# Kernel optimization log

Hardware: AMD Instinct MI355X
Metric: run time of the kernel (lower is better)

The kernel has to match this reference:

```python
import jax, jax.numpy as jnp
import numpy as np

K = 4096   # infeatures
N = 11008  # outfeatures
T = 8192   # tokens (batch*seq)
GROUP = 32
E8M0_BIAS = 127
E2M1_VALS = jnp.array([0.0, 0.5, 1.0, 1.5, 2.0, 3.0, 4.0, 6.0], dtype=jnp.float32)


def setup_inputs() -> dict:
    key = jax.random.key(0)
    k1, k2, k3, k4 = jax.random.split(key, 4)
    x = jax.random.normal(k1, (T, K), dtype=jnp.float32)
    # packed fp4: 8 nibbles per int32 along the in-feature axis -> [K//8, N]
    weight_packed = jax.random.randint(k2, (K // 8, N), 0, 2147483647, dtype=jnp.int32)
    # e8m0 exponents near the bias so 2^(e-127) stays well-conditioned in fp32
    weight_scale_e8m0 = 112 + jax.random.randint(k3, (K // GROUP, N), 0, 30, dtype=jnp.int32)
    bias = jax.random.normal(k4, (N,), dtype=jnp.float32)
    return {"x": x, "weight_packed": weight_packed,
            "weight_scale_e8m0": weight_scale_e8m0, "bias": bias}


def dequantize_weight(weight_packed, weight_scale_e8m0):
    # unpack 8 fp4 nibbles per int32: nibble j -> in-feature row r*8 + j
    shifts = (jnp.arange(8, dtype=jnp.int32) * 4)[None, :, None]       # [1,8,1]
    nib = (weight_packed[:, None, :] >> shifts) & 0xF                   # [K//8,8,N]
    mag = E2M1_VALS[nib & 0x7]                                           # e2m1 magnitude
    sign = jnp.where((nib >> 3) & 1 == 1, -1.0, 1.0).astype(jnp.float32)
    w = (mag * sign).reshape(K, N)
    # per-group e8m0 scale: 2^(e - 127), groups of 32 along in-features
    scale = jnp.exp2((weight_scale_e8m0 - E8M0_BIAS).astype(jnp.float32))  # [K//32,N]
    w = (w.reshape(K // GROUP, GROUP, N) * scale[:, None, :]).reshape(K, N)
    return w


def reference(x, weight_packed, weight_scale_e8m0, bias):
    w = dequantize_weight(weight_packed, weight_scale_e8m0)  # [K, N]
    return x @ w + bias                                       # [T, N]
```

## Files before the change

kernel.cpp:

```cpp
#include <hip/hip_runtime.h>


#define TDIM 8192
#define KDIM 4096
#define NDIM 11008

typedef __attribute__((ext_vector_type(8))) short short8;
typedef __attribute__((ext_vector_type(8))) unsigned short ushort8;
typedef __attribute__((ext_vector_type(4))) float f32x4;

__device__ __forceinline__ unsigned short f2bf(float f) {
    unsigned int u = __float_as_uint(f);
    u += 0x7FFFu + ((u >> 16) & 1u);
    return (unsigned short)(u >> 16);
}

__device__ __forceinline__ unsigned short nib2bf(unsigned int v, int e) {
    unsigned int m3 = v & 7u;
    if (m3 == 0u) return 0;
    unsigned int s = (v & 8u) << 12;
    unsigned int E = (unsigned int)e + (m3 >> 1) - 1u;
    unsigned int man = (m3 >= 2u) ? ((m3 & 1u) << 6) : 0u;
    return (unsigned short)(s | (E << 7) | man);
}

__device__ __forceinline__ void gload_lds16(const void* g, void* l) {
    __builtin_amdgcn_global_load_lds(
        (const __attribute__((address_space(1))) void*)g,
        (__attribute__((address_space(3))) void*)l, 16, 0, 0);
}

__global__ __launch_bounds__(256) void convert_x(const float* __restrict__ x,
                                                 unsigned short* __restrict__ xbf) {
    size_t i = ((size_t)blockIdx.x * 256 + threadIdx.x) * 8;
    float4 v0 = *(const float4*)(x + i);
    float4 v1 = *(const float4*)(x + i + 4);
    ushort8 r;
    r[0] = f2bf(v0.x); r[1] = f2bf(v0.y); r[2] = f2bf(v0.z); r[3] = f2bf(v0.w);
    r[4] = f2bf(v1.x); r[5] = f2bf(v1.y); r[6] = f2bf(v1.z); r[7] = f2bf(v1.w);
    *(ushort8*)(xbf + i) = r;
}

__global__ __launch_bounds__(256) void dequant_w(const int* __restrict__ wp,
                                                 const int* __restrict__ wse,
                                                 unsigned short* __restrict__ wt) {
    __shared__ int sT[64][65];
    const int tid = threadIdx.x;
    const int n0 = blockIdx.x * 64;
    const int r0 = blockIdx.y * 64;

    #pragma unroll
    for (int i = 0; i < 16; ++i) {
        int idx = i * 256 + tid;
        int r = idx >> 6, n = idx & 63;
        sT[r][n] = wp[(size_t)(r0 + r) * NDIM + n0 + n];
    }
    __syncthreads();
    #pragma unroll
    for (int i = 0; i < 16; ++i) {
        int idx = i * 256 + tid;
        int n = idx >> 6, r = idx & 63;
        unsigned int p = (unsigned int)sT[r][n];
        int e = wse[(size_t)((r0 + r) >> 2) * NDIM + n0 + n];
        ushort8 o;
        #pragma unroll
        for (int j = 0; j < 8; ++j) o[j] = nib2bf((p >> (4 * j)) & 0xFu, e);
        *(ushort8*)(wt + (size_t)(n0 + n) * KDIM + (size_t)(r0 + r) * 8) = o;
    }
}

__global__ __launch_bounds__(512, 1) void gemm256(const unsigned short* __restrict__ xbf,
                                                  const unsigned short* __restrict__ wt,
                                                  const float* __restrict__ bias,
                                                  float* __restrict__ out) {
    __shared__ __attribute__((aligned(16))) unsigned short lds[2][2][16384];
    const int tid = threadIdx.x;
    const int l = tid & 63, wid = tid >> 6;
    const int wm = wid >> 2, wn = wid & 3;

    {
    }
    int b = blockIdx.x;
    int swz = (b & 7) * 172 + (b >> 3);
    int band = swz / 344;
    int r = swz % 344;
    int st = r >> 5; if (st > 10) st = 10;
    int ii = r - (st << 5);
    int w = (st < 10) ? 4 : 3;
    const int bm0 = (band * 8 + ii / w) * 256;
    const int bn0 = (st * 4 + ii % w) * 256;

    int r_s[2], k_s[2];
    #pragma unroll
    for (int j = 0; j < 2; ++j) {
        int chunk = j * 512 + wid * 64 + l;
        int sr = chunk >> 6;
        int cin = chunk & 63;
        cin ^= ((cin >> 5) & 1) << 1;
        r_s[j] = sr * 16 + (cin >> 2);
        k_s[j] = (cin & 3) * 8;
    }

    f32x4 acc[8][4] = {};
    short8 afr[4], bfr[4];

    auto stage = [&](int s) {
        int tau = s >> 2;
        int idx = s & 3;
        int mat = idx & 1, hk = idx >> 1, c = tau & 1;
        const unsigned short* base = mat ? wt : xbf;
        int rb = mat ? bn0 : bm0;
        int kb = tau * 64 + hk * 32;
        #pragma unroll
        for (int j = 0; j < 2; ++j) {
            const unsigned short* src = base + (size_t)(rb + r_s[j]) * KDIM + kb + k_s[j];
            unsigned short* dst = &lds[c][mat][hk * 8192 + (j * 512 + wid * 64) * 8];
            gload_lds16(src, dst);
        }
    };

    #pragma unroll
    for (int s = 0; s < 6; ++s) stage(s);
    asm volatile("s_waitcnt vmcnt(4)" ::: "memory");
    __builtin_amdgcn_s_barrier();

    #pragma unroll 2
    for (int t = 0; t < 64; ++t) {
        const unsigned short* tA = &lds[t & 1][0][0];
        const unsigned short* tB = &lds[t & 1][1][0];
        #pragma unroll
        for (int p = 0; p < 4; ++p) {
            const int ks = p >> 1, mh = p & 1;
            if (mh == 0) {
                #pragma unroll
                for (int nf = 0; nf < 4; ++nf) {
                    int byte = ks * 16384 + (wn * 4 + nf) * 1024 + (l & 15) * 64 + ((l >> 4) << 4);
                    byte ^= (l & 8) << 2;
                    bfr[nf] = *(const short8*)((const char*)tB + byte);
                }
            }
            #pragma unroll
            for (int i = 0; i < 4; ++i) {
                int byte = ks * 16384 + (wm * 8 + mh * 4 + i) * 1024 + (l & 15) * 64 + ((l >> 4) << 4);
                byte ^= (l & 8) << 2;
                afr[i] = *(const short8*)((const char*)tA + byte);
            }
            int s = 4 * t + p + 6;
            if (s < 256) stage(s);
            __builtin_amdgcn_s_barrier();
            asm volatile("s_waitcnt lgkmcnt(0)" ::: "memory");
            __builtin_amdgcn_s_setprio(1);
            #pragma unroll
            for (int i = 0; i < 4; ++i)
                #pragma unroll
                for (int nf = 0; nf < 4; ++nf)
                    acc[mh * 4 + i][nf] = __builtin_amdgcn_mfma_f32_16x16x32_bf16(
                        afr[i], bfr[nf], acc[mh * 4 + i][nf], 0, 0, 0);
            __builtin_amdgcn_s_setprio(0);
            if (p == 3) {
                if (t < 62) asm volatile("s_waitcnt vmcnt(4)" ::: "memory");
                else        asm volatile("s_waitcnt vmcnt(0)" ::: "memory");
            }
            __builtin_amdgcn_s_barrier();
        }
    }

    const int crow = (l >> 4) * 4, ccol = l & 15;
    #pragma unroll
    for (int nf = 0; nf < 4; ++nf) {
        int col = bn0 + wn * 64 + nf * 16 + ccol;
        float bv = bias[col];
        #pragma unroll
        for (int m = 0; m < 8; ++m) {
            int row0 = bm0 + wm * 128 + m * 16 + crow;
            #pragma unroll
            for (int j2 = 0; j2 < 4; ++j2)
                __builtin_nontemporal_store(acc[m][nf][j2] + bv,
                                            &out[(size_t)(row0 + j2) * NDIM + col]);
        }
    }
}

__global__ __launch_bounds__(256, 2) void gemm_fused(const float* __restrict__ x,
                                                     const int* __restrict__ wp,
                                                     const int* __restrict__ wse,
                                                     const float* __restrict__ bias,
                                                     float* __restrict__ out) {
    __shared__ __attribute__((aligned(16))) unsigned short lA[128 * 64];
    __shared__ __attribute__((aligned(16))) unsigned short lB[128 * 64];
    const int tid = threadIdx.x;
    const int l = tid & 63, wid = tid >> 6;
    const int bn0 = blockIdx.x * 128, bm0 = blockIdx.y * 128;
    const int wm = wid >> 1, wn = wid & 1;

    f32x4 acc[4][4] = {};

    for (int k0 = 0; k0 < KDIM; k0 += 64) {
        float4 av0[4], av1[4];
        unsigned int bp[4];
        int be[4];
        #pragma unroll
        for (int i = 0; i < 4; ++i) {
            int seg = i * 256 + tid;
            int row = seg >> 3, kseg = seg & 7;
            const float4* p = (const float4*)(x + (size_t)(bm0 + row) * KDIM + k0 + kseg * 8);
            av0[i] = p[0]; av1[i] = p[1];
        }
        #pragma unroll
        for (int i = 0; i < 4; ++i) {
            int idx = i * 256 + tid;
            int ln = idx & 127, lr = idx >> 7;
            bp[i] = ((const unsigned int*)wp)[(size_t)(k0 / 8 + lr) * NDIM + bn0 + ln];
            be[i] = wse[(size_t)((k0 + lr * 8) >> 5) * NDIM + bn0 + ln];
        }
        #pragma unroll
        for (int i = 0; i < 4; ++i) {
            int seg = i * 256 + tid;
            int row = seg >> 3, kseg = seg & 7;
            ushort8 r;
            r[0] = f2bf(av0[i].x); r[1] = f2bf(av0[i].y); r[2] = f2bf(av0[i].z); r[3] = f2bf(av0[i].w);
            r[4] = f2bf(av1[i].x); r[5] = f2bf(av1[i].y); r[6] = f2bf(av1[i].z); r[7] = f2bf(av1[i].w);
            *(ushort8*)&lA[row * 64 + kseg * 8] = r;
        }
        #pragma unroll
        for (int i = 0; i < 4; ++i) {
            int idx = i * 256 + tid;
            int ln = idx & 127, lr = idx >> 7;
            unsigned int p = bp[i];
            int e = be[i];
            ushort8 r;
            #pragma unroll
            for (int j = 0; j < 8; ++j) r[j] = nib2bf((p >> (4 * j)) & 0xFu, e);
            *(ushort8*)&lB[ln * 64 + lr * 8] = r;
        }
        __syncthreads();
        #pragma unroll
        for (int kc = 0; kc < 2; ++kc) {
            short8 a[4], b[4];
            #pragma unroll
            for (int f = 0; f < 4; ++f) {
                a[f] = *(const short8*)&lA[(wm * 64 + f * 16 + (l & 15)) * 64 + kc * 32 + (l >> 4) * 8];
                b[f] = *(const short8*)&lB[(wn * 64 + f * 16 + (l & 15)) * 64 + kc * 32 + (l >> 4) * 8];
            }
            #pragma unroll
            for (int fm = 0; fm < 4; ++fm)
                #pragma unroll
                for (int fn = 0; fn < 4; ++fn)
                    acc[fm][fn] = __builtin_amdgcn_mfma_f32_16x16x32_bf16(a[fm], b[fn], acc[fm][fn], 0, 0, 0);
        }
        __syncthreads();
    }

    const int crow = (l >> 4) * 4, ccol = l & 15;
    #pragma unroll
    for (int fn = 0; fn < 4; ++fn) {
        int col = bn0 + wn * 64 + fn * 16 + ccol;
        float bv = bias[col];
        #pragma unroll
        for (int fm = 0; fm < 4; ++fm) {
            int row0 = bm0 + wm * 64 + fm * 16 + crow;
            #pragma unroll
            for (int j = 0; j < 4; ++j)
                out[(size_t)(row0 + j) * NDIM + col] = acc[fm][fn][j] + bv;
        }
    }
}

extern "C" void kernel_launch(void* const* d_in, const int* in_sizes, int n_in,
                              void* d_out, int out_size, void* d_ws, size_t ws_size,
                              hipStream_t stream) {
    (void)in_sizes; (void)n_in; (void)out_size;
    const float* x = (const float*)d_in[0];
    const int* wp = (const int*)d_in[1];
    const int* wse = (const int*)d_in[2];
    const float* bias = (const float*)d_in[3];
    float* out = (float*)d_out;

    const size_t xbf_bytes = (size_t)TDIM * KDIM * 2;
    const size_t wt_bytes = (size_t)NDIM * KDIM * 2;

    if (ws_size >= xbf_bytes + wt_bytes) {
        unsigned short* xbf = (unsigned short*)d_ws;
        unsigned short* wt = (unsigned short*)((char*)d_ws + xbf_bytes);
        hipLaunchKernelGGL(convert_x, dim3((TDIM * KDIM) / (256 * 8)), dim3(256), 0, stream, x, xbf);
        hipLaunchKernelGGL(dequant_w, dim3(NDIM / 64, (KDIM / 8) / 64), dim3(256), 0, stream, wp, wse, wt);
        hipLaunchKernelGGL(gemm256, dim3((NDIM / 256) * (TDIM / 256)), dim3(512), 0, stream, xbf, wt, bias, out);
    } else {
        hipLaunchKernelGGL(gemm_fused, dim3(NDIM / 128, TDIM / 128), dim3(256), 0, stream, x, wp, wse, bias, out);
    }
}
```

Measured before the change: 737.6 us.

## Double-buffer MFMA fragments in registers to overlap LDS reads with compute

Restructures the main GEMM loop so LDS fragment reads for the next MFMA cluster are issued while the current cluster runs, using ping-pong A/B register fragments. It also cuts the barriers from two per sub-step to two per K-tile and prefetches the next tile's first fragments before the loop-end barrier. This aims to hide LDS latency and reduce synchronization stalls, at the cost of more VGPRs and a more delicate ordering of waitcnt and barriers against the async global-to-LDS stages.

```diff
diff --git a/kernel.cpp b/kernel.cpp
--- a/kernel.cpp
+++ b/kernel.cpp
@@ -78,8 +78,6 @@
     const int l = tid & 63, wid = tid >> 6;
     const int wm = wid >> 2, wn = wid & 3;
 
-    {
-    }
     int b = blockIdx.x;
     int swz = (b & 7) * 172 + (b >> 3);
     int band = swz / 344;
@@ -102,9 +100,10 @@
     }
 
     f32x4 acc[8][4] = {};
-    short8 afr[4], bfr[4];
+    short8 bfr0[4], bfr1[4], afrA[4], afrB[4];
 
     auto stage = [&](int s) {
+        if (s >= 256) return;
         int tau = s >> 2;
         int idx = s & 3;
         int mat = idx & 1, hk = idx >> 1, c = tau & 1;
@@ -119,50 +118,70 @@
         }
     };
 
+    const int lbyte = (((l & 15) * 64 + ((l >> 4) << 4))) ^ ((l & 8) << 2);
+
+    auto readA = [&](const unsigned short* base, int ks, int mh, short8* dst) {
+        #pragma unroll
+        for (int i = 0; i < 4; ++i)
+            dst[i] = *(const short8*)((const char*)base + ks * 16384 +
+                                      (wm * 8 + mh * 4 + i) * 1024 + lbyte);
+    };
+    auto readB = [&](const unsigned short* base, int ks, short8* dst) {
+        #pragma unroll
+        for (int nf = 0; nf < 4; ++nf)
+            dst[nf] = *(const short8*)((const char*)base + ks * 16384 +
+                                       (wn * 4 + nf) * 1024 + lbyte);
+    };
+    auto cluster = [&](short8* a, short8* bf, int mh) {
+        __builtin_amdgcn_s_setprio(1);
+        #pragma unroll
+        for (int i = 0; i < 4; ++i)
+            #pragma unroll
+            for (int nf = 0; nf < 4; ++nf)
+                acc[mh * 4 + i][nf] = __builtin_amdgcn_mfma_f32_16x16x32_bf16(
+                    a[i], bf[nf], acc[mh * 4 + i][nf], 0, 0, 0);
+        __builtin_amdgcn_s_setprio(0);
+    };
+
     #pragma unroll
     for (int s = 0; s < 6; ++s) stage(s);
     asm volatile("s_waitcnt vmcnt(4)" ::: "memory");
     __builtin_amdgcn_s_barrier();
+    readB(&lds[0][1][0], 0, bfr0);
+    readA(&lds[0][0][0], 0, 0, afrA);
 
     #pragma unroll 2
     for (int t = 0; t < 64; ++t) {
-        const unsigned short* tA = &lds[t & 1][0][0];
-        const unsigned short* tB = &lds[t & 1][1][0];
-        #pragma unroll
-        for (int p = 0; p < 4; ++p) {
-            const int ks = p >> 1, mh = p & 1;
-            if (mh == 0) {
-                #pragma unroll
-                for (int nf = 0; nf < 4; ++nf) {
-                    int byte = ks * 16384 + (wn * 4 + nf) * 1024 + (l & 15) * 64 + ((l >> 4) << 4);
-                    byte ^= (l & 8) << 2;
-                    bfr[nf] = *(const short8*)((const char*)tB + byte);
-                }
-            }
-            #pragma unroll
-            for (int i = 0; i < 4; ++i) {
-                int byte = ks * 16384 + (wm * 8 + mh * 4 + i) * 1024 + (l & 15) * 64 + ((l >> 4) << 4);
-                byte ^= (l & 8) << 2;
-                afr[i] = *(const short8*)((const char*)tA + byte);
-            }
-            int s = 4 * t + p + 6;
-            if (s < 256) stage(s);
-            __builtin_amdgcn_s_barrier();
-            asm volatile("s_waitcnt lgkmcnt(0)" ::: "memory");
-            __builtin_amdgcn_s_setprio(1);
-            #pragma unroll
-            for (int i = 0; i < 4; ++i)
-                #pragma unroll
-                for (int nf = 0; nf < 4; ++nf)
-                    acc[mh * 4 + i][nf] = __builtin_amdgcn_mfma_f32_16x16x32_bf16(
-                        afr[i], bfr[nf], acc[mh * 4 + i][nf], 0, 0, 0);
-            __builtin_amdgcn_s_setprio(0);
-            if (p == 3) {
-                if (t < 62) asm volatile("s_waitcnt vmcnt(4)" ::: "memory");
-                else        asm volatile("s_waitcnt vmcnt(0)" ::: "memory");
-            }
-            __builtin_amdgcn_s_barrier();
-        }
+        const int c = t & 1;
+        const unsigned short* tA = &lds[c][0][0];
+        const unsigned short* tB = &lds[c][1][0];
+        const unsigned short* nA = &lds[c ^ 1][0][0];
+        const unsigned short* nB = &lds[c ^ 1][1][0];
+
+        stage(4 * t + 6);
+        readA(tA, 0, 1, afrB);
+        cluster(afrA, bfr0, 0);
+
+        stage(4 * t + 7);
+        readB(tB, 1, bfr1);
+        readA(tA, 1, 0, afrA);
+        cluster(afrB, bfr0, 1);
+        if (t < 63) asm volatile("s_waitcnt vmcnt(4)" ::: "memory");
+        __builtin_amdgcn_s_barrier();
+
+        stage(4 * t + 8);
+        readA(tA, 1, 1, afrB);
+        cluster(afrA, bfr1, 0);
+
+        stage(4 * t + 9);
+        if (t < 63) {
+            readB(nB, 0, bfr0);
+            readA(nA, 0, 0, afrA);
+        }
+        cluster(afrB, bfr1, 1);
+        if (t < 62)       asm volatile("s_waitcnt vmcnt(4)" ::: "memory");
+        else if (t == 62) asm volatile("s_waitcnt vmcnt(0)" ::: "memory");
+        __builtin_amdgcn_s_barrier();
     }
 
     const int crow = (l >> 4) * 4, ccol = l & 15;
@@ -236,17 +255,17 @@
         __syncthreads();
         #pragma unroll
         for (int kc = 0; kc < 2; ++kc) {
-            short8 a[4], b[4];
+            short8 a[4], bb[4];
             #pragma unroll
             for (int f = 0; f < 4; ++f) {
                 a[f] = *(const short8*)&lA[(wm * 64 + f * 16 + (l & 15)) * 64 + kc * 32 + (l >> 4) * 8];
-                b[f] = *(const short8*)&lB[(wn * 64 + f * 16 + (l & 15)) * 64 + kc * 32 + (l >> 4) * 8];
+                bb[f] = *(const short8*)&lB[(wn * 64 + f * 16 + (l & 15)) * 64 + kc * 32 + (l >> 4) * 8];
             }
             #pragma unroll
             for (int fm = 0; fm < 4; ++fm)
                 #pragma unroll
                 for (int fn = 0; fn < 4; ++fn)
-                    acc[fm][fn] = __builtin_amdgcn_mfma_f32_16x16x32_bf16(a[fm], b[fn], acc[fm][fn], 0, 0, 0);
+                    acc[fm][fn] = __builtin_amdgcn_mfma_f32_16x16x32_bf16(a[fm], bb[fn], acc[fm][fn], 0, 0, 0);
         }
         __syncthreads();
     }
```

Result: slower. 1.803 ms (+144.5%).

## Software-pipeline LDS fragment reads against MFMA clusters with ping-pong registers

Applied to the files above, without the earlier changes.

Rewrites the main GEMM loop as a hand-scheduled macro body. Fragments for the next MFMA cluster are read from LDS into alternate register sets (aX/aY, bX/bY) while the current cluster runs. Barriers drop from four to two per k-step, and global loads use precomputed pointers advanced incrementally. The goal is to hide LDS latency and cut barrier and address overhead. In exchange it uses more VGPRs and makes the async-load and barrier ordering more fragile.

```diff
diff --git a/kernel.cpp b/kernel.cpp
--- a/kernel.cpp
+++ b/kernel.cpp
@@ -69,6 +69,64 @@
     }
 }
 
+#define STG(PJ0, PJ1, GOFF, C, MAT, HK)                                        \
+    do {                                                                       \
+        gload_lds16((PJ0) + (GOFF), ldsW + (C)*32768 + (MAT)*16384 + (HK)*8192);           \
+        gload_lds16((PJ1) + (GOFF), ldsW + (C)*32768 + (MAT)*16384 + (HK)*8192 + 4096);    \
+    } while (0)
+
+#define RD_A(CB, KS, MH, DST)                                                                  \
+    DST[0] = *(const short8*)(ldsC + (CB)*65536 + (KS)*16384 + ((MH)*4 + 0)*1024 + aoff);      \
+    DST[1] = *(const short8*)(ldsC + (CB)*65536 + (KS)*16384 + ((MH)*4 + 1)*1024 + aoff);      \
+    DST[2] = *(const short8*)(ldsC + (CB)*65536 + (KS)*16384 + ((MH)*4 + 2)*1024 + aoff);      \
+    DST[3] = *(const short8*)(ldsC + (CB)*65536 + (KS)*16384 + ((MH)*4 + 3)*1024 + aoff);
+
+#define RD_B(CB, KS, DST)                                                                      \
+    DST[0] = *(const short8*)(ldsC + (CB)*65536 + 32768 + (KS)*16384 + 0*1024 + boff);         \
+    DST[1] = *(const short8*)(ldsC + (CB)*65536 + 32768 + (KS)*16384 + 1*1024 + boff);         \
+    DST[2] = *(const short8*)(ldsC + (CB)*65536 + 32768 + (KS)*16384 + 2*1024 + boff);         \
+    DST[3] = *(const short8*)(ldsC + (CB)*65536 + 32768 + (KS)*16384 + 3*1024 + boff);
+
+#define CLUSTER(A, B, MH)                                                      \
+    __builtin_amdgcn_s_setprio(1);                                             \
+    _Pragma("unroll")                                                          \
+    for (int i_ = 0; i_ < 4; ++i_) {                                           \
+        _Pragma("unroll")                                                      \
+        for (int n_ = 0; n_ < 4; ++n_)                                         \
+            acc[(MH)*4 + i_][n_] = __builtin_amdgcn_mfma_f32_16x16x32_bf16(    \
+                A[i_], B[n_], acc[(MH)*4 + i_][n_], 0, 0, 0);                  \
+    }                                                                          \
+    __builtin_amdgcn_s_setprio(0);
+
+#define BODY(T, C)                                                             \
+    do {                                                                       \
+                       \
+        if ((T) < 63) STG(pA0, pA1, 96, (C)^1, 0, 1);                          \
+        RD_A((C), 0, 1, aY)                                                    \
+        CLUSTER(aX, bX, 0)                                                     \
+                \
+        if ((T) < 63) STG(pB0, pB1, 96, (C)^1, 1, 1);                          \
+        RD_B((C), 1, bY)                                                       \
+        RD_A((C), 1, 0, aX)                                                    \
+        CLUSTER(aY, bX, 1)                                                     \
+        \
+        if ((T) < 63) asm volatile("s_waitcnt vmcnt(4)" ::: "memory");         \
+        __builtin_amdgcn_s_barrier();                                          \
+               \
+        if ((T) < 62) STG(pA0, pA1, 128, (C), 0, 0);                           \
+        RD_A((C), 1, 1, aY)                                                    \
+        CLUSTER(aX, bY, 0)                                                     \
+                       \
+        if ((T) < 62) STG(pB0, pB1, 128, (C), 1, 0);                           \
+        if ((T) < 63) { RD_B((C)^1, 0, bX) RD_A((C)^1, 0, 0, aX) }             \
+        CLUSTER(aY, bY, 1)                                                     \
+            \
+        if ((T) < 62)       asm volatile("s_waitcnt vmcnt(4)" ::: "memory");   \
+        else if ((T) == 62) asm volatile("s_waitcnt vmcnt(0)" ::: "memory");   \
+        __builtin_amdgcn_s_barrier();                                          \
+        pA0 += 64; pA1 += 64; pB0 += 64; pB1 += 64;                            \
+    } while (0)
+
 __global__ __launch_bounds__(512, 1) void gemm256(const unsigned short* __restrict__ xbf,
                                                   const unsigned short* __restrict__ wt,
                                                   const float* __restrict__ bias,
@@ -78,8 +136,6 @@
     const int l = tid & 63, wid = tid >> 6;
     const int wm = wid >> 2, wn = wid & 3;
 
-    {
-    }
     int b = blockIdx.x;
     int swz = (b & 7) * 172 + (b >> 3);
     int band = swz / 344;
@@ -90,79 +146,50 @@
     const int bm0 = (band * 8 + ii / w) * 256;
     const int bn0 = (st * 4 + ii % w) * 256;
 
-    int r_s[2], k_s[2];
-    #pragma unroll
-    for (int j = 0; j < 2; ++j) {
-        int chunk = j * 512 + wid * 64 + l;
-        int sr = chunk >> 6;
+    int rs0, ks0, rs1, ks1;
+    {
+        int chunk = wid * 64 + l;
         int cin = chunk & 63;
         cin ^= ((cin >> 5) & 1) << 1;
-        r_s[j] = sr * 16 + (cin >> 2);
-        k_s[j] = (cin & 3) * 8;
-    }
+        rs0 = (chunk >> 6) * 16 + (cin >> 2);
+        ks0 = (cin & 3) * 8;
+        chunk = 512 + wid * 64 + l;
+        cin = chunk & 63;
+        cin ^= ((cin >> 5) & 1) << 1;
+        rs1 = (chunk >> 6) * 16 + (cin >> 2);
+        ks1 = (cin & 3) * 8;
+    }
+
+    const unsigned short* pA0 = xbf + (size_t)(bm0 + rs0) * KDIM + ks0;
+    const unsigned short* pA1 = xbf + (size_t)(bm0 + rs1) * KDIM + ks1;
+    const unsigned short* pB0 = wt + (size_t)(bn0 + rs0) * KDIM + ks0;
+    const unsigned short* pB1 = wt + (size_t)(bn0 + rs1) * KDIM + ks1;
+
+    unsigned short* ldsW = &lds[0][0][0] + wid * 512;
+    const char* ldsC = (const char*)&lds[0][0][0];
+
+    const int lbyte = (((l & 15) * 64 + ((l >> 4) << 4))) ^ ((l & 8) << 2);
+    const int aoff = wm * 8192 + lbyte;
+    const int boff = wn * 4096 + lbyte;
 
     f32x4 acc[8][4] = {};
-    short8 afr[4], bfr[4];
-
-    auto stage = [&](int s) {
-        int tau = s >> 2;
-        int idx = s & 3;
-        int mat = idx & 1, hk = idx >> 1, c = tau & 1;
-        const unsigned short* base = mat ? wt : xbf;
-        int rb = mat ? bn0 : bm0;
-        int kb = tau * 64 + hk * 32;
-        #pragma unroll
-        for (int j = 0; j < 2; ++j) {
-            const unsigned short* src = base + (size_t)(rb + r_s[j]) * KDIM + kb + k_s[j];
-            unsigned short* dst = &lds[c][mat][hk * 8192 + (j * 512 + wid * 64) * 8];
-            gload_lds16(src, dst);
-        }
-    };
-
-    #pragma unroll
-    for (int s = 0; s < 6; ++s) stage(s);
+    short8 aX[4], aY[4], bX[4], bY[4];
+
+    STG(pA0, pA1, 0, 0, 0, 0);
+    STG(pB0, pB1, 0, 0, 1, 0);
+    STG(pA0, pA1, 32, 0, 0, 1);
+    STG(pB0, pB1, 32, 0, 1, 1);
+    STG(pA0, pA1, 64, 1, 0, 0);
+    STG(pB0, pB1, 64, 1, 1, 0);
     asm volatile("s_waitcnt vmcnt(4)" ::: "memory");
     __builtin_amdgcn_s_barrier();
-
-    #pragma unroll 2
-    for (int t = 0; t < 64; ++t) {
-        const unsigned short* tA = &lds[t & 1][0][0];
-        const unsigned short* tB = &lds[t & 1][1][0];
-        #pragma unroll
-        for (int p = 0; p < 4; ++p) {
-            const int ks = p >> 1, mh = p & 1;
-            if (mh == 0) {
-                #pragma unroll
-                for (int nf = 0; nf < 4; ++nf) {
-                    int byte = ks * 16384 + (wn * 4 + nf) * 1024 + (l & 15) * 64 + ((l >> 4) << 4);
-                    byte ^= (l & 8) << 2;
-                    bfr[nf] = *(const short8*)((const char*)tB + byte);
-                }
-            }
-            #pragma unroll
-            for (int i = 0; i < 4; ++i) {
-                int byte = ks * 16384 + (wm * 8 + mh * 4 + i) * 1024 + (l & 15) * 64 + ((l >> 4) << 4);
-                byte ^= (l & 8) << 2;
-                afr[i] = *(const short8*)((const char*)tA + byte);
-            }
-            int s = 4 * t + p + 6;
-            if (s < 256) stage(s);
-            __builtin_amdgcn_s_barrier();
-            asm volatile("s_waitcnt lgkmcnt(0)" ::: "memory");
-            __builtin_amdgcn_s_setprio(1);
-            #pragma unroll
-            for (int i = 0; i < 4; ++i)
-                #pragma unroll
-                for (int nf = 0; nf < 4; ++nf)
-                    acc[mh * 4 + i][nf] = __builtin_amdgcn_mfma_f32_16x16x32_bf16(
-                        afr[i], bfr[nf], acc[mh * 4 + i][nf], 0, 0, 0);
-            __builtin_amdgcn_s_setprio(0);
-            if (p == 3) {
-                if (t < 62) asm volatile("s_waitcnt vmcnt(4)" ::: "memory");
-                else        asm volatile("s_waitcnt vmcnt(0)" ::: "memory");
-            }
-            __builtin_amdgcn_s_barrier();
-        }
+    RD_B(0, 0, bX)
+    RD_A(0, 0, 0, aX)
+
+    for (int tt = 0; tt < 32; ++tt) {
+        const int ta = 2 * tt;
+        BODY(ta, 0);
+        BODY(ta + 1, 1);
     }
 
     const int crow = (l >> 4) * 4, ccol = l & 15;
@@ -236,17 +263,17 @@
         __syncthreads();
         #pragma unroll
         for (int kc = 0; kc < 2; ++kc) {
-            short8 a[4], b[4];
+            short8 a[4], bb[4];
             #pragma unroll
             for (int f = 0; f < 4; ++f) {
                 a[f] = *(const short8*)&lA[(wm * 64 + f * 16 + (l & 15)) * 64 + kc * 32 + (l >> 4) * 8];
-                b[f] = *(const short8*)&lB[(wn * 64 + f * 16 + (l & 15)) * 64 + kc * 32 + (l >> 4) * 8];
+                bb[f] = *(const short8*)&lB[(wn * 64 + f * 16 + (l & 15)) * 64 + kc * 32 + (l >> 4) * 8];
             }
             #pragma unroll
             for (int fm = 0; fm < 4; ++fm)
                 #pragma unroll
                 for (int fn = 0; fn < 4; ++fn)
-                    acc[fm][fn] = __builtin_amdgcn_mfma_f32_16x16x32_bf16(a[fm], b[fn], acc[fm][fn], 0, 0, 0);
+                    acc[fm][fn] = __builtin_amdgcn_mfma_f32_16x16x32_bf16(a[fm], bb[fn], acc[fm][fn], 0, 0, 0);
         }
         __syncthreads();
     }
```

After: 688.1 us. -6.7%, faster.
